# Kernel optimization log

Hardware: AMD Instinct MI355X
Metric: run time of the kernel (lower is better)

The kernel has to match this reference:

```python
import jax, jax.numpy as jnp
import numpy as np

NUM_EMB = 100000
BASE_DIM = 32
DIMS = [32, 32, 32, 51, 102]  # max(32*2**i//5, 32)
BATCH, SEQ = 512, 2048


def setup_inputs() -> dict:
    key = jax.random.key(0)
    ks = jax.random.split(key, 10)
    inp = {}
    inp["x"] = jax.random.randint(ks[0], (BATCH, SEQ), 0, NUM_EMB)
    inp["bucket_assignment"] = jax.random.randint(ks[1], (NUM_EMB,), 0, 5)
    for i, d in enumerate(DIMS):
        t = jax.random.normal(ks[2 + i], (NUM_EMB, d), dtype=jnp.float32)
        inp[f"emb{i}"] = t.at[0].set(0.0)  # padding_idx=0
    # Linear layers for buckets 3 and 4 (dims 51 and 102 -> 32); stored as [in, out]
    inp["W3"] = jax.random.normal(ks[7], (51, BASE_DIM), dtype=jnp.float32) * (1.0 / np.sqrt(51))
    inp["b3"] = jnp.zeros((BASE_DIM,), dtype=jnp.float32)
    inp["W4"] = jax.random.normal(ks[8], (102, BASE_DIM), dtype=jnp.float32) * (1.0 / np.sqrt(102))
    inp["b4"] = jnp.zeros((BASE_DIM,), dtype=jnp.float32)
    return inp


def reference(x, bucket_assignment, emb0, emb1, emb2, emb3, emb4, W3, b3, W4, b4):
    batch_shape = x.shape
    xf = x.reshape(-1)                      # [T]
    bk = bucket_assignment[xf]              # [T] bucket id per token
    # per-bucket lookup (+ projection for buckets with dim != base_dim)
    o0 = emb0[xf]                           # [T, 32] identity projection
    o1 = emb1[xf]
    o2 = emb2[xf]
    o3 = emb3[xf] @ W3 + b3                 # [T, 32]
    o4 = emb4[xf] @ W4 + b4                 # [T, 32]
    # buckets are mutually exclusive -> masked sum == masked scatter
    m = jax.nn.one_hot(bk, 5, dtype=jnp.float32)  # [T, 5]
    out = (o0 * m[:, 0:1] + o1 * m[:, 1:2] + o2 * m[:, 2:3]
           + o3 * m[:, 3:4] + o4 * m[:, 4:5])
    return out.reshape(*batch_shape, BASE_DIM)
```

## Files before the change

kernel.cpp:

```cpp
#include <hip/hip_runtime.h>


#define NUM_EMB_C 100000
#define BASE_DIM_C 32

__global__ __launch_bounds__(256) void fae_build_table(
    const int* __restrict__ bucket,
    const float* __restrict__ e0, const float* __restrict__ e1,
    const float* __restrict__ e2, const float* __restrict__ e3,
    const float* __restrict__ e4,
    const float* __restrict__ W3, const float* __restrict__ b3,
    const float* __restrict__ W4, const float* __restrict__ b4,
    float* __restrict__ tbl, int num_emb)
{
    __shared__ float w3[51 * 32];
    __shared__ float w4[102 * 32];
    for (int i = threadIdx.x; i < 51 * 32; i += 256) w3[i] = W3[i];
    for (int i = threadIdx.x; i < 102 * 32; i += 256) w4[i] = W4[i];
    __syncthreads();

    const int lane = threadIdx.x & 31;
    const int grp  = threadIdx.x >> 5;
    const int e = blockIdx.x * 8 + grp;
    if (e >= num_emb) return;

    const int bk = bucket[e];
    float val;
    if (bk == 0) {
        val = e0[(size_t)e * 32 + lane];
    } else if (bk == 1) {
        val = e1[(size_t)e * 32 + lane];
    } else if (bk == 2) {
        val = e2[(size_t)e * 32 + lane];
    } else if (bk == 3) {
        const float* row = e3 + (size_t)e * 51;
        float h0 = row[lane];
        float h1 = (lane < 19) ? row[32 + lane] : 0.f;
        float acc = b3[lane];
        #pragma unroll
        for (int k = 0; k < 32; ++k)
            acc = fmaf(__shfl(h0, k, 32), w3[k * 32 + lane], acc);
        #pragma unroll
        for (int k = 0; k < 19; ++k)
            acc = fmaf(__shfl(h1, k, 32), w3[(32 + k) * 32 + lane], acc);
        val = acc;
    } else {
        const float* row = e4 + (size_t)e * 102;
        float h0 = row[lane];
        float h1 = row[32 + lane];
        float h2 = row[64 + lane];
        float h3 = (lane < 6) ? row[96 + lane] : 0.f;
        float acc = b4[lane];
        #pragma unroll
        for (int k = 0; k < 32; ++k)
            acc = fmaf(__shfl(h0, k, 32), w4[k * 32 + lane], acc);
        #pragma unroll
        for (int k = 0; k < 32; ++k)
            acc = fmaf(__shfl(h1, k, 32), w4[(32 + k) * 32 + lane], acc);
        #pragma unroll
        for (int k = 0; k < 32; ++k)
            acc = fmaf(__shfl(h2, k, 32), w4[(64 + k) * 32 + lane], acc);
        #pragma unroll
        for (int k = 0; k < 6; ++k)
            acc = fmaf(__shfl(h3, k, 32), w4[(96 + k) * 32 + lane], acc);
        val = acc;
    }
    tbl[(size_t)e * 32 + lane] = val;
}

__global__ __launch_bounds__(256) void fae_gather(
    const int* __restrict__ x, const float4* __restrict__ tbl,
    float4* __restrict__ out, int n4)
{
    int gid = blockIdx.x * 256 + threadIdx.x;
    if (gid >= n4) return;
    int xi = x[gid >> 3];
    out[gid] = tbl[(size_t)xi * 8 + (gid & 7)];
}

extern "C" void kernel_launch(void* const* d_in, const int* in_sizes, int n_in,
                              void* d_out, int out_size, void* d_ws, size_t ws_size,
                              hipStream_t stream) {
    const int*   x      = (const int*)d_in[0];
    const int*   bucket = (const int*)d_in[1];
    const float* e0     = (const float*)d_in[2];
    const float* e1     = (const float*)d_in[3];
    const float* e2     = (const float*)d_in[4];
    const float* e3     = (const float*)d_in[5];
    const float* e4     = (const float*)d_in[6];
    const float* W3     = (const float*)d_in[7];
    const float* b3     = (const float*)d_in[8];
    const float* W4     = (const float*)d_in[9];
    const float* b4     = (const float*)d_in[10];

    const int num_emb = in_sizes[1];
    float* tbl = (float*)d_ws;

    int build_blocks = (num_emb + 7) / 8;
    fae_build_table<<<build_blocks, 256, 0, stream>>>(
        bucket, e0, e1, e2, e3, e4, W3, b3, W4, b4, tbl, num_emb);

    int n4 = out_size / 4;
    int gather_blocks = (n4 + 255) / 256;
    fae_gather<<<gather_blocks, 256, 0, stream>>>(
        x, (const float4*)tbl, (float4*)d_out, n4);
}
```

Measured before the change: 309.5 us.

## Restructure table build with register-resident weights and nontemporal gather stores

```diff
diff --git a/kernel.cpp b/kernel.cpp
--- a/kernel.cpp
+++ b/kernel.cpp
@@ -1,10 +1,9 @@
 #include <hip/hip_runtime.h>
 
 
-#define NUM_EMB_C 100000
-#define BASE_DIM_C 32
+typedef float f32x4 __attribute__((ext_vector_type(4)));
 
-__global__ __launch_bounds__(256) void fae_build_table(
+__global__ __launch_bounds__(256) void fae_build_v2(
     const int* __restrict__ bucket,
     const float* __restrict__ e0, const float* __restrict__ e1,
     const float* __restrict__ e2, const float* __restrict__ e3,
@@ -13,69 +12,70 @@
     const float* __restrict__ W4, const float* __restrict__ b4,
     float* __restrict__ tbl, int num_emb)
 {
-    __shared__ float w3[51 * 32];
-    __shared__ float w4[102 * 32];
-    for (int i = threadIdx.x; i < 51 * 32; i += 256) w3[i] = W3[i];
-    for (int i = threadIdx.x; i < 102 * 32; i += 256) w4[i] = W4[i];
-    __syncthreads();
+    const int lane = threadIdx.x & 63;
+    const int d    = lane & 31;
+    const int h    = lane >> 5;
+    int wid = (int)(blockIdx.x * (blockDim.x >> 6) + (threadIdx.x >> 6));
+    wid = __builtin_amdgcn_readfirstlane(wid);
+    const int nw = (int)(gridDim.x * (blockDim.x >> 6));
 
-    const int lane = threadIdx.x & 31;
-    const int grp  = threadIdx.x >> 5;
-    const int e = blockIdx.x * 8 + grp;
-    if (e >= num_emb) return;
+    float w4r[51];
+#pragma unroll
+    for (int j = 0; j < 51; ++j) w4r[j] = W4[(h * 51 + j) * 32 + d];
+    float w3r[26];
+#pragma unroll
+    for (int j = 0; j < 26; ++j) {
+        int k = h * 26 + j;
+        w3r[j] = (k < 51) ? W3[k * 32 + d] : 0.0f;
+    }
+    const float bias3 = b3[d];
+    const float bias4 = b4[d];
 
-    const int bk = bucket[e];
-    float val;
-    if (bk == 0) {
-        val = e0[(size_t)e * 32 + lane];
-    } else if (bk == 1) {
-        val = e1[(size_t)e * 32 + lane];
-    } else if (bk == 2) {
-        val = e2[(size_t)e * 32 + lane];
-    } else if (bk == 3) {
-        const float* row = e3 + (size_t)e * 51;
-        float h0 = row[lane];
-        float h1 = (lane < 19) ? row[32 + lane] : 0.f;
-        float acc = b3[lane];
-        #pragma unroll
-        for (int k = 0; k < 32; ++k)
-            acc = fmaf(__shfl(h0, k, 32), w3[k * 32 + lane], acc);
-        #pragma unroll
-        for (int k = 0; k < 19; ++k)
-            acc = fmaf(__shfl(h1, k, 32), w3[(32 + k) * 32 + lane], acc);
-        val = acc;
-    } else {
-        const float* row = e4 + (size_t)e * 102;
-        float h0 = row[lane];
-        float h1 = row[32 + lane];
-        float h2 = row[64 + lane];
-        float h3 = (lane < 6) ? row[96 + lane] : 0.f;
-        float acc = b4[lane];
-        #pragma unroll
-        for (int k = 0; k < 32; ++k)
-            acc = fmaf(__shfl(h0, k, 32), w4[k * 32 + lane], acc);
-        #pragma unroll
-        for (int k = 0; k < 32; ++k)
-            acc = fmaf(__shfl(h1, k, 32), w4[(32 + k) * 32 + lane], acc);
-        #pragma unroll
-        for (int k = 0; k < 32; ++k)
-            acc = fmaf(__shfl(h2, k, 32), w4[(64 + k) * 32 + lane], acc);
-        #pragma unroll
-        for (int k = 0; k < 6; ++k)
-            acc = fmaf(__shfl(h3, k, 32), w4[(96 + k) * 32 + lane], acc);
-        val = acc;
+    for (int e = wid; e < num_emb; e += nw) {
+        const int bk = __builtin_amdgcn_readfirstlane(bucket[e]);
+        if (bk < 3) {
+            const float* src = (bk == 0) ? e0 : (bk == 1) ? e1 : e2;
+            if (h == 0) tbl[(size_t)e * 32 + d] = src[(size_t)e * 32 + d];
+        } else if (bk == 3) {
+            const float* row = e3 + (size_t)e * 51 + h * 26;
+            float a0 = h ? 0.0f : bias3;
+            float a1 = 0.0f;
+#pragma unroll
+            for (int j = 0; j < 26; ++j) {
+                int jj = (h && (j == 25)) ? 24 : j;
+                float rv = row[jj];
+                if (j & 1) a1 = fmaf(rv, w3r[j], a1);
+                else       a0 = fmaf(rv, w3r[j], a0);
+            }
+            float acc = a0 + a1;
+            acc += __shfl_xor(acc, 32, 64);
+            if (h == 0) tbl[(size_t)e * 32 + d] = acc;
+        } else {
+            const float* row = e4 + (size_t)e * 102 + h * 51;
+            float a0 = h ? 0.0f : bias4;
+            float a1 = 0.0f;
+#pragma unroll
+            for (int j = 0; j < 51; ++j) {
+                float rv = row[j];
+                if (j & 1) a1 = fmaf(rv, w4r[j], a1);
+                else       a0 = fmaf(rv, w4r[j], a0);
+            }
+            float acc = a0 + a1;
+            acc += __shfl_xor(acc, 32, 64);
+            if (h == 0) tbl[(size_t)e * 32 + d] = acc;
+        }
     }
-    tbl[(size_t)e * 32 + lane] = val;
 }
 
 __global__ __launch_bounds__(256) void fae_gather(
-    const int* __restrict__ x, const float4* __restrict__ tbl,
-    float4* __restrict__ out, int n4)
+    const int* __restrict__ x, const f32x4* __restrict__ tbl,
+    f32x4* __restrict__ out, int n4)
 {
     int gid = blockIdx.x * 256 + threadIdx.x;
     if (gid >= n4) return;
     int xi = x[gid >> 3];
-    out[gid] = tbl[(size_t)xi * 8 + (gid & 7)];
+    f32x4 v = tbl[(size_t)xi * 8 + (gid & 7)];
+    __builtin_nontemporal_store(v, out + gid);
 }
 
 extern "C" void kernel_launch(void* const* d_in, const int* in_sizes, int n_in,
@@ -96,12 +96,11 @@
     const int num_emb = in_sizes[1];
     float* tbl = (float*)d_ws;
 
-    int build_blocks = (num_emb + 7) / 8;
-    fae_build_table<<<build_blocks, 256, 0, stream>>>(
+    fae_build_v2<<<1024, 256, 0, stream>>>(
         bucket, e0, e1, e2, e3, e4, W3, b3, W4, b4, tbl, num_emb);
 
     int n4 = out_size / 4;
     int gather_blocks = (n4 + 255) / 256;
     fae_gather<<<gather_blocks, 256, 0, stream>>>(
-        x, (const float4*)tbl, (float4*)d_out, n4);
+        x, (const f32x4*)tbl, (f32x4*)d_out, n4);
 }
```

Result: faster. 262.9 us (-15.0%).
